# Optimization experiments

Measured on AMD Instinct MI355X. Metric: run time of the kernel, lower is better.

Reference implementation:

```python
import jax, jax.numpy as jnp
import numpy as np

N_NODES = 100000
N_EDGES = 640000


def _sage_conv(x, src, dst, w_agg, b, w_root, n_nodes):
    # mean aggregation of source features into destination nodes
    msgs = x[src]  # [E, D] gather
    summed = jax.ops.segment_sum(msgs, dst, num_segments=n_nodes)  # [N, D]
    deg = jax.ops.segment_sum(jnp.ones((src.shape[0],), dtype=x.dtype), dst,
                              num_segments=n_nodes)  # [N]
    mean = summed / jnp.clip(deg, 1.0)[:, None]  # isolated nodes -> 0
    # PyG SAGEConv: lin_l(agg) + lin_r(x); bias lives on lin_l
    return mean @ w_agg.T + b + x @ w_root.T


def setup_inputs() -> dict:
    key = jax.random.key(0)
    ks = jax.random.split(key, 8)
    d_in, d_hid, d_out = 128, 256, 64
    x = jax.random.normal(ks[0], (N_NODES, d_in), dtype=jnp.float32)
    edge_index = jax.random.randint(ks[1], (2, N_EDGES), 0, N_NODES, dtype=jnp.int64)
    s = 0.05
    return {
        "x": x,
        "edge_index": edge_index,
        "w1_agg": jax.random.normal(ks[2], (d_hid, d_in), dtype=jnp.float32) * s,
        "b1": jax.random.normal(ks[3], (d_hid,), dtype=jnp.float32) * s,
        "w1_root": jax.random.normal(ks[4], (d_hid, d_in), dtype=jnp.float32) * s,
        "w2_agg": jax.random.normal(ks[5], (d_out, d_hid), dtype=jnp.float32) * s,
        "b2": jax.random.normal(ks[6], (d_out,), dtype=jnp.float32) * s,
        "w2_root": jax.random.normal(ks[7], (d_out, d_hid), dtype=jnp.float32) * s,
    }


def reference(x, edge_index, w1_agg, b1, w1_root, w2_agg, b2, w2_root):
    src, dst = edge_index[0], edge_index[1]
    n = x.shape[0]
    h = _sage_conv(x, src, dst, w1_agg, b1, w1_root, n)
    h = jax.nn.relu(h)
    # dropout(p=0.5) is identity in eval mode
    h = _sage_conv(h, src, dst, w2_agg, b2, w2_root, n)
    return jax.nn.log_softmax(h, axis=1)
```

## Files before the change

kernel.cpp:

```cpp
#include <hip/hip_runtime.h>

#define N_NODES 100000
#define N_EDGES 640000
#define D_IN 128
#define D_HID 256
#define D_OUT 64

#define NROWPAD 100096
#define CAP 32

#define OB_CNT      0u
#define OB_BUCKET   401408u
#define OB_XQ       13201408u
#define OB_MEANQ    26013696u
#define OB_HB       38825984u
#define OB_ZRB      90075136u
#define OB_ZAQ      102887424u
#define OB_WCAT1    109293568u
#define OB_WCAT2    109424640u

typedef __attribute__((ext_vector_type(8))) short bf16x8;
typedef __attribute__((ext_vector_type(4))) float f32x4;
typedef __attribute__((ext_vector_type(2))) float f32x2;

__device__ __forceinline__ ushort f2bf(float f) {
    uint u = __float_as_uint(f);
    u += 0x7FFFu + ((u >> 16) & 1u);
    return (ushort)(u >> 16);
}
__device__ __forceinline__ float bf1(ushort u) { return __uint_as_float((uint)u << 16); }
__device__ __forceinline__ uchar f2q(float v) {
    return (uchar)(__builtin_amdgcn_cvt_pk_fp8_f32(v, v, 0, false) & 0xFF);
}
__device__ __forceinline__ uint pk8(float4 v) {
    uint q = (uint)__builtin_amdgcn_cvt_pk_fp8_f32(v.x, v.y, 0, false);
    return (uint)__builtin_amdgcn_cvt_pk_fp8_f32(v.z, v.w, (int)q, true);
}
__device__ __forceinline__ uint pkbf(float lo, float hi) {
    return (__float_as_uint(lo) >> 16) | (__float_as_uint(hi) & 0xFFFF0000u);
}


__global__ __launch_bounds__(256) void k_z(
    int* __restrict__ cnt,
    const float* __restrict__ w1a, const float* __restrict__ w1r,
    const float* __restrict__ w2r, const float* __restrict__ w2a,
    ushort* __restrict__ wcat1, ushort* __restrict__ wcat2)
{
    int b = blockIdx.x;
    if (b < 98) {
        int i = (b * 256 + threadIdx.x) * 4;
        *(int4*)(cnt + i) = make_int4(0, 0, 0, 0);
    } else {
        int i = (b - 98) * 256 + threadIdx.x;
        if (i < 65536) {
            int n = i >> 8, k = i & 255;
            float v = (k < 128) ? w1a[n * 128 + k] : w1r[n * 128 + (k - 128)];
            wcat1[i] = f2bf(v);
        } else {
            int j = i - 65536;
            int n = j >> 8, k = j & 255;
            float v = (n < 64) ? w2r[n * 256 + k] : w2a[(n - 64) * 256 + k];
            wcat2[j] = f2bf(v);
        }
    }
}


__global__ __launch_bounds__(256) void k_fc(
    const int* __restrict__ src, const int* __restrict__ dst,
    int* __restrict__ cnt, int* __restrict__ bucket,
    const float* __restrict__ x, uchar* __restrict__ xq)
{
    int b = blockIdx.x;
    if (b < 625) {
        int e = (b * 256 + threadIdx.x) * 4;
        int4 d = *(const int4*)(dst + e);
        int4 sv = *(const int4*)(src + e);
        int p0 = atomicAdd(&cnt[d.x], 1);
        int p1 = atomicAdd(&cnt[d.y], 1);
        int p2 = atomicAdd(&cnt[d.z], 1);
        int p3 = atomicAdd(&cnt[d.w], 1);
        if (p0 < CAP) bucket[(d.x << 5) + p0] = sv.x;
        if (p1 < CAP) bucket[(d.y << 5) + p1] = sv.y;
        if (p2 < CAP) bucket[(d.z << 5) + p2] = sv.z;
        if (p3 < CAP) bucket[(d.w << 5) + p3] = sv.w;
    } else {
        size_t i = ((size_t)(b - 625) * 256 + threadIdx.x) * 16;
        float4 v0 = *(const float4*)(x + i);
        float4 v1 = *(const float4*)(x + i + 4);
        float4 v2 = *(const float4*)(x + i + 8);
        float4 v3 = *(const float4*)(x + i + 12);
        uint4 q;
        q.x = pk8(v0); q.y = pk8(v1); q.z = pk8(v2); q.w = pk8(v3);
        *(uint4*)(xq + i) = q;
    }
}


__global__ __launch_bounds__(256) void k_gather(
    const uchar* __restrict__ xq, const int* __restrict__ cnt,
    const int* __restrict__ bucket, uchar* __restrict__ meanq)
{
    int tid = threadIdx.x;
    int node = blockIdx.x * 8 + (tid >> 5);
    int l = tid & 31;
    int g = l & 3, t = l >> 2;
    int nraw = cnt[node];
    int n = min(nraw, CAP);
    const int* cs = bucket + (node << 5);

    float a[16] = {};
    for (int j = 0; j < n; j += 4) {
        int jj = j + g;
        int ii = (jj < n) ? jj : 0;
        float w = (jj < n) ? 1.0f : 0.0f;
        int s = cs[ii];
        uint4 q = *(const uint4*)(xq + (size_t)s * D_IN + t * 16);
        f32x2 p;
        p = __builtin_amdgcn_cvt_pk_f32_fp8(q.x, false); a[0] += w*p.x; a[1] += w*p.y;
        p = __builtin_amdgcn_cvt_pk_f32_fp8(q.x, true);  a[2] += w*p.x; a[3] += w*p.y;
        p = __builtin_amdgcn_cvt_pk_f32_fp8(q.y, false); a[4] += w*p.x; a[5] += w*p.y;
        p = __builtin_amdgcn_cvt_pk_f32_fp8(q.y, true);  a[6] += w*p.x; a[7] += w*p.y;
        p = __builtin_amdgcn_cvt_pk_f32_fp8(q.z, false); a[8] += w*p.x; a[9] += w*p.y;
        p = __builtin_amdgcn_cvt_pk_f32_fp8(q.z, true);  a[10]+= w*p.x; a[11]+= w*p.y;
        p = __builtin_amdgcn_cvt_pk_f32_fp8(q.w, false); a[12]+= w*p.x; a[13]+= w*p.y;
        p = __builtin_amdgcn_cvt_pk_f32_fp8(q.w, true);  a[14]+= w*p.x; a[15]+= w*p.y;
    }

    float b[8];
    #pragma unroll
    for (int j = 0; j < 8; ++j) {
        int base = (j & 3) + 8 * (j >> 2);
        float mine = (l & 1) ? a[base + 4] : a[base];
        float send = (l & 1) ? a[base]     : a[base + 4];
        b[j] = mine + __shfl_xor(send, 1);
    }
    float c[4];
    #pragma unroll
    for (int j = 0; j < 4; ++j) {
        float mine = (l & 2) ? b[j + 4] : b[j];
        float send = (l & 2) ? b[j]     : b[j + 4];
        c[j] = mine + __shfl_xor(send, 2);
    }
    float id = 1.0f / fmaxf((float)nraw, 1.0f);
    uint q = (uint)__builtin_amdgcn_cvt_pk_fp8_f32(c[0] * id, c[1] * id, 0, false);
    q = (uint)__builtin_amdgcn_cvt_pk_fp8_f32(c[2] * id, c[3] * id, (int)q, true);
    *(uint*)(meanq + (size_t)node * D_IN + t * 16 + (l & 3) * 4) = q;
}


template<int MODE>
__global__ __launch_bounds__(256, 2) void k_gemm(
    const void* __restrict__ A0v, const void* __restrict__ A1v,
    const ushort* __restrict__ B,
    const float* __restrict__ bias,
    void* __restrict__ out0, void* __restrict__ out1)
{
    __shared__ char lds[32 * 1024];
    const int BB = (MODE == 0) ? 8192 : 16384;

    const int tid = threadIdx.x;
    const int lane = tid & 63;
    const int w = tid >> 6;
    const int wm = w >> 1, wn = w & 1;
    const int row0 = blockIdx.x * 128;
    const int col0 = blockIdx.y * 128;

    f32x4 acc[4][4] = {};

    for (int kt = 0; kt < 4; ++kt) {
        const int k0 = kt * 64;

        if (MODE == 0) {
            const uchar* asrc = (kt < 2) ? (const uchar*)A0v : (const uchar*)A1v;
            int kbyte = (kt & 1) * 64;
            #pragma unroll
            for (int i = 0; i < 2; ++i) {
                int elem = i * 256 + tid;
                int r = elem >> 2;
                int c4 = (elem & 3) ^ (r & 3);
                const uchar* gp = asrc + (size_t)(row0 + r) * 128 + kbyte + c4 * 16;
                __builtin_amdgcn_global_load_lds(
                    (const __attribute__((address_space(1))) void*)gp,
                    (__attribute__((address_space(3))) void*)&lds[i * 4096 + w * 1024],
                    16, 0, 0);
            }
        } else {
            const ushort* asrc = (const ushort*)A0v;
            #pragma unroll
            for (int i = 0; i < 4; ++i) {
                int elem = i * 256 + tid;
                int r = elem >> 3;
                int c8 = (elem & 7) ^ (r & 7);
                const ushort* gp = asrc + (size_t)(row0 + r) * 256 + k0 + c8 * 8;
                __builtin_amdgcn_global_load_lds(
                    (const __attribute__((address_space(1))) void*)gp,
                    (__attribute__((address_space(3))) void*)&lds[i * 4096 + w * 1024],
                    16, 0, 0);
            }
        }
        #pragma unroll
        for (int i = 0; i < 4; ++i) {
            int elem = i * 256 + tid;
            int r = elem >> 3;
            int c8 = (elem & 7) ^ (r & 7);
            const ushort* gp = B + (size_t)(col0 + r) * 256 + k0 + c8 * 8;
            __builtin_amdgcn_global_load_lds(
                (const __attribute__((address_space(1))) void*)gp,
                (__attribute__((address_space(3))) void*)&lds[BB + i * 4096 + w * 1024],
                16, 0, 0);
        }
        asm volatile("s_waitcnt vmcnt(0)" ::: "memory");
        __syncthreads();

        #pragma unroll
        for (int ks = 0; ks < 2; ++ks) {
            bf16x8 af[4], bfr[4];
            #pragma unroll
            for (int mi = 0; mi < 4; ++mi) {
                int r = wm * 64 + mi * 16 + (lane & 15);
                int g = lane >> 4;
                if (MODE == 0) {
                    int c4l = ks * 2 + (g >> 1);
                    int abyte = r * 64 + ((c4l ^ (r & 3)) << 4) + ((g & 1) << 3);
                    uint2 q = *(const uint2*)(lds + abyte);
                    f32x2 p0 = __builtin_amdgcn_cvt_pk_f32_fp8(q.x, false);
                    f32x2 p1 = __builtin_amdgcn_cvt_pk_f32_fp8(q.x, true);
                    f32x2 p2 = __builtin_amdgcn_cvt_pk_f32_fp8(q.y, false);
                    f32x2 p3 = __builtin_amdgcn_cvt_pk_f32_fp8(q.y, true);
                    uint4 u;
                    u.x = pkbf(p0.x, p0.y); u.y = pkbf(p1.x, p1.y);
                    u.z = pkbf(p2.x, p2.y); u.w = pkbf(p3.x, p3.y);
                    af[mi] = *(bf16x8*)&u;
                } else {
                    int c8 = ks * 4 + g;
                    int abyte = r * 128 + ((c8 ^ (r & 7)) << 4);
                    af[mi] = *(const bf16x8*)(lds + abyte);
                }
            }
            #pragma unroll
            for (int ni = 0; ni < 4; ++ni) {
                int r = wn * 64 + ni * 16 + (lane & 15);
                int c8 = ks * 4 + (lane >> 4);
                int byteoff = BB + r * 128 + ((c8 ^ (r & 7)) << 4);
                bfr[ni] = *(const bf16x8*)(lds + byteoff);
            }
            #pragma unroll
            for (int mi = 0; mi < 4; ++mi)
                #pragma unroll
                for (int ni = 0; ni < 4; ++ni)
                    acc[mi][ni] = __builtin_amdgcn_mfma_f32_16x16x32_bf16(
                        af[mi], bfr[ni], acc[mi][ni], 0, 0, 0);
        }
        __syncthreads();
    }

    const int orow_base = row0 + wm * 64;
    const int ocol_base = col0 + wn * 64;
    #pragma unroll
    for (int mi = 0; mi < 4; ++mi) {
        #pragma unroll
        for (int ni = 0; ni < 4; ++ni) {
            int ocol = ocol_base + ni * 16 + (lane & 15);
            #pragma unroll
            for (int r = 0; r < 4; ++r) {
                int orow = orow_base + mi * 16 + (lane >> 4) * 4 + r;
                float v = acc[mi][ni][r];
                if (MODE == 0) {
                    v = fmaxf(v + bias[ocol], 0.0f);
                    ((ushort*)out0)[(size_t)orow * 256 + ocol] = f2bf(v);
                } else {
                    if (ocol < 64)
                        ((ushort*)out0)[(size_t)orow * 64 + ocol] = f2bf(v + bias[ocol]);
                    else
                        ((uchar*)out1)[(size_t)orow * 64 + (ocol - 64)] = f2q(v);
                }
            }
        }
    }
}


__global__ __launch_bounds__(256) void k_final(
    const ushort* __restrict__ zrb, const uchar* __restrict__ zaq,
    const int* __restrict__ cnt, const int* __restrict__ bucket,
    float* __restrict__ out)
{
    int tid = threadIdx.x;
    int lane = tid & 63;
    int l = lane & 31;
    int node = blockIdx.x * 8 + (tid >> 5);
    int g = l & 7, t = l >> 3;
    int nraw = cnt[node];
    int n = min(nraw, CAP);
    const int* cs = bucket + (node << 5);

    float a[16] = {};
    for (int j = 0; j < n; j += 8) {
        int jj = j + g;
        int ii = (jj < n) ? jj : 0;
        float w = (jj < n) ? 1.0f : 0.0f;
        int s = cs[ii];
        uint4 q = *(const uint4*)(zaq + (size_t)s * 64 + t * 16);
        f32x2 p;
        p = __builtin_amdgcn_cvt_pk_f32_fp8(q.x, false); a[0] += w*p.x; a[1] += w*p.y;
        p = __builtin_amdgcn_cvt_pk_f32_fp8(q.x, true);  a[2] += w*p.x; a[3] += w*p.y;
        p = __builtin_amdgcn_cvt_pk_f32_fp8(q.y, false); a[4] += w*p.x; a[5] += w*p.y;
        p = __builtin_amdgcn_cvt_pk_f32_fp8(q.y, true);  a[6] += w*p.x; a[7] += w*p.y;
        p = __builtin_amdgcn_cvt_pk_f32_fp8(q.z, false); a[8] += w*p.x; a[9] += w*p.y;
        p = __builtin_amdgcn_cvt_pk_f32_fp8(q.z, true);  a[10]+= w*p.x; a[11]+= w*p.y;
        p = __builtin_amdgcn_cvt_pk_f32_fp8(q.w, false); a[12]+= w*p.x; a[13]+= w*p.y;
        p = __builtin_amdgcn_cvt_pk_f32_fp8(q.w, true);  a[14]+= w*p.x; a[15]+= w*p.y;
    }

    float b[8];
    #pragma unroll
    for (int j = 0; j < 8; ++j) {
        float mine = (l & 1) ? a[2*j+1] : a[2*j];
        float send = (l & 1) ? a[2*j]   : a[2*j+1];
        b[j] = mine + __shfl_xor(send, 1);
    }
    float c[4];
    #pragma unroll
    for (int j = 0; j < 4; ++j) {
        float mine = (l & 2) ? b[2*j+1] : b[2*j];
        float send = (l & 2) ? b[2*j]   : b[2*j+1];
        c[j] = mine + __shfl_xor(send, 2);
    }
    float m0 = (l & 4) ? c[1] : c[0];
    float s0 = (l & 4) ? c[0] : c[1];
    float e0 = m0 + __shfl_xor(s0, 4);
    float m1 = (l & 4) ? c[3] : c[2];
    float s1 = (l & 4) ? c[2] : c[3];
    float e1 = m1 + __shfl_xor(s1, 4);

    int c0 = t * 16 + (l & 7);
    float id = 1.0f / fmaxf((float)nraw, 1.0f);
    float v0 = e0 * id + bf1(zrb[(size_t)node * 64 + c0]);
    float v1 = e1 * id + bf1(zrb[(size_t)node * 64 + c0 + 8]);

    float m = fmaxf(v0, v1);
    #pragma unroll
    for (int o = 1; o < 32; o <<= 1) m = fmaxf(m, __shfl_xor(m, o));
    float ssum = __expf(v0 - m) + __expf(v1 - m);
    #pragma unroll
    for (int o = 1; o < 32; o <<= 1) ssum += __shfl_xor(ssum, o);
    float lse = m + __logf(ssum);

    out[(size_t)node * 64 + c0]     = v0 - lse;
    out[(size_t)node * 64 + c0 + 8] = v1 - lse;
}


extern "C" void kernel_launch(void* const* d_in, const int* in_sizes, int n_in,
                              void* d_out, int out_size, void* d_ws, size_t ws_size,
                              hipStream_t stream)
{
    const float* x   = (const float*)d_in[0];
    const int*   ei  = (const int*)d_in[1];
    const float* w1a = (const float*)d_in[2];
    const float* b1  = (const float*)d_in[3];
    const float* w1r = (const float*)d_in[4];
    const float* w2a = (const float*)d_in[5];
    const float* b2  = (const float*)d_in[6];
    const float* w2r = (const float*)d_in[7];
    float* out = (float*)d_out;

    char* ws = (char*)d_ws;
    const int* src = ei;
    const int* dst = ei + N_EDGES;

    int*    cnt       = (int*)(ws + OB_CNT);
    int*    bucket    = (int*)(ws + OB_BUCKET);
    uchar*  xq        = (uchar*)(ws + OB_XQ);
    uchar*  meanq     = (uchar*)(ws + OB_MEANQ);
    ushort* hb        = (ushort*)(ws + OB_HB);
    ushort* zrb       = (ushort*)(ws + OB_ZRB);
    uchar*  zaq       = (uchar*)(ws + OB_ZAQ);
    ushort* wcat1     = (ushort*)(ws + OB_WCAT1);
    ushort* wcat2     = (ushort*)(ws + OB_WCAT2);

    k_z<<<482, 256, 0, stream>>>(cnt, w1a, w1r, w2r, w2a, wcat1, wcat2);
    k_fc<<<3750, 256, 0, stream>>>(src, dst, cnt, bucket, x, xq);

    k_gather<<<12500, 256, 0, stream>>>(xq, cnt, bucket, meanq);

    dim3 g1(NROWPAD / 128, 2);
    k_gemm<0><<<g1, 256, 0, stream>>>((const void*)meanq, (const void*)xq,
                                      wcat1, b1, (void*)hb, nullptr);

    dim3 g2(NROWPAD / 128, 1);
    k_gemm<1><<<g2, 256, 0, stream>>>((const void*)hb, (const void*)hb,
                                      wcat2, b2, (void*)zrb, (void*)zaq);

    k_final<<<12500, 256, 0, stream>>>(zrb, zaq, cnt, bucket, out);
}
```

Baseline: 147.7 us.

## Transform-before-aggregate in layer 1, fusing bucket build into the first GEMM

Layer 1 now multiplies x by both weight matrices first, producing a 512-column output: root half in bf16 with bias, aggregate half in fp8. The mean aggregation then runs on the projected 256-wide fp8 features and fuses bias-added root, ReLU and the bf16 store of h. The edge bucketing atomics are folded into the GEMM kernel, which also reads fp32 x directly, dropping the separate x quantise pass and the layer-1 gather and GEMM launches. The cost is a gather over 256-wide rows instead of 128, plus more intermediate traffic for the 512-wide projection.

```diff
diff --git a/kernel.cpp b/kernel.cpp
--- a/kernel.cpp
+++ b/kernel.cpp
@@ -4,20 +4,19 @@
 #define N_EDGES 640000
 #define D_IN 128
 #define D_HID 256
-#define D_OUT 64
 
 #define NROWPAD 100096
 #define CAP 32
 
 #define OB_CNT      0u
 #define OB_BUCKET   401408u
-#define OB_XQ       13201408u
-#define OB_MEANQ    26013696u
-#define OB_HB       38825984u
-#define OB_ZRB      90075136u
-#define OB_ZAQ      102887424u
-#define OB_WCAT1    109293568u
-#define OB_WCAT2    109424640u
+#define OB_Z1R      13201408u
+#define OB_Z1A      64450560u
+#define OB_HB       90075136u
+#define OB_ZRB      141324288u
+#define OB_ZAQ      154136576u
+#define OB_WCAT1    160542720u
+#define OB_WCAT2    160673792u
 
 typedef __attribute__((ext_vector_type(8))) short bf16x8;
 typedef __attribute__((ext_vector_type(4))) float f32x4;
@@ -32,10 +31,6 @@
 __device__ __forceinline__ uchar f2q(float v) {
     return (uchar)(__builtin_amdgcn_cvt_pk_fp8_f32(v, v, 0, false) & 0xFF);
 }
-__device__ __forceinline__ uint pk8(float4 v) {
-    uint q = (uint)__builtin_amdgcn_cvt_pk_fp8_f32(v.x, v.y, 0, false);
-    return (uint)__builtin_amdgcn_cvt_pk_fp8_f32(v.z, v.w, (int)q, true);
-}
 __device__ __forceinline__ uint pkbf(float lo, float hi) {
     return (__float_as_uint(lo) >> 16) | (__float_as_uint(hi) & 0xFFFF0000u);
 }
@@ -43,7 +38,7 @@
 
 __global__ __launch_bounds__(256) void k_z(
     int* __restrict__ cnt,
-    const float* __restrict__ w1a, const float* __restrict__ w1r,
+    const float* __restrict__ w1r, const float* __restrict__ w1a,
     const float* __restrict__ w2r, const float* __restrict__ w2a,
     ushort* __restrict__ wcat1, ushort* __restrict__ wcat2)
 {
@@ -54,8 +49,8 @@
     } else {
         int i = (b - 98) * 256 + threadIdx.x;
         if (i < 65536) {
-            int n = i >> 8, k = i & 255;
-            float v = (k < 128) ? w1a[n * 128 + k] : w1r[n * 128 + (k - 128)];
+            int n = i >> 7, k = i & 127;
+            float v = (n < 256) ? w1r[n * 128 + k] : w1a[(n - 256) * 128 + k];
             wcat1[i] = f2bf(v);
         } else {
             int j = i - 65536;
@@ -67,45 +62,127 @@
 }
 
 
-__global__ __launch_bounds__(256) void k_fc(
+__global__ __launch_bounds__(256, 2) void k_big(
     const int* __restrict__ src, const int* __restrict__ dst,
     int* __restrict__ cnt, int* __restrict__ bucket,
-    const float* __restrict__ x, uchar* __restrict__ xq)
-{
-    int b = blockIdx.x;
-    if (b < 625) {
-        int e = (b * 256 + threadIdx.x) * 4;
-        int4 d = *(const int4*)(dst + e);
-        int4 sv = *(const int4*)(src + e);
-        int p0 = atomicAdd(&cnt[d.x], 1);
-        int p1 = atomicAdd(&cnt[d.y], 1);
-        int p2 = atomicAdd(&cnt[d.z], 1);
-        int p3 = atomicAdd(&cnt[d.w], 1);
-        if (p0 < CAP) bucket[(d.x << 5) + p0] = sv.x;
-        if (p1 < CAP) bucket[(d.y << 5) + p1] = sv.y;
-        if (p2 < CAP) bucket[(d.z << 5) + p2] = sv.z;
-        if (p3 < CAP) bucket[(d.w << 5) + p3] = sv.w;
-    } else {
-        size_t i = ((size_t)(b - 625) * 256 + threadIdx.x) * 16;
-        float4 v0 = *(const float4*)(x + i);
-        float4 v1 = *(const float4*)(x + i + 4);
-        float4 v2 = *(const float4*)(x + i + 8);
-        float4 v3 = *(const float4*)(x + i + 12);
-        uint4 q;
-        q.x = pk8(v0); q.y = pk8(v1); q.z = pk8(v2); q.w = pk8(v3);
-        *(uint4*)(xq + i) = q;
-    }
-}
-
-
-__global__ __launch_bounds__(256) void k_gather(
-    const uchar* __restrict__ xq, const int* __restrict__ cnt,
-    const int* __restrict__ bucket, uchar* __restrict__ meanq)
+    const float* __restrict__ x, const ushort* __restrict__ wcat1,
+    const float* __restrict__ b1,
+    ushort* __restrict__ z1r, uchar* __restrict__ z1a)
+{
+    __shared__ char lds[49152];
+
+    const int bb = blockIdx.x;
+    const int tid = threadIdx.x;
+
+    int e = bb * 205 + tid;
+    bool edge_ok = (tid < 205) && (e < N_EDGES);
+    int ed = edge_ok ? dst[e] : 0;
+    int es = edge_ok ? src[e] : 0;
+
+    const int bx = bb >> 2, by = bb & 3;
+    const int row0 = bx * 128;
+    const int col0 = by * 128;
+    const int lane = tid & 63;
+    const int w = tid >> 6;
+    const int wm = w >> 1, wn = w & 1;
+
+    f32x4 acc[4][4] = {};
+
+    for (int kt = 0; kt < 2; ++kt) {
+        #pragma unroll
+        for (int i = 0; i < 8; ++i) {
+            int elem = i * 256 + tid;
+            int r = elem >> 4;
+            int c = elem & 15;
+            int csrc = c ^ ((r & 7) << 1);
+            int rr = row0 + r; rr = rr < N_NODES ? rr : (N_NODES - 1);
+            const float* gp = x + (size_t)rr * 128 + kt * 64 + csrc * 4;
+            __builtin_amdgcn_global_load_lds(
+                (const __attribute__((address_space(1))) void*)gp,
+                (__attribute__((address_space(3))) void*)&lds[i * 4096 + w * 1024],
+                16, 0, 0);
+        }
+        #pragma unroll
+        for (int i = 0; i < 4; ++i) {
+            int elem = i * 256 + tid;
+            int r = elem >> 3;
+            int c8 = (elem & 7) ^ (r & 7);
+            const ushort* gp = wcat1 + (size_t)(col0 + r) * 128 + kt * 64 + c8 * 8;
+            __builtin_amdgcn_global_load_lds(
+                (const __attribute__((address_space(1))) void*)gp,
+                (__attribute__((address_space(3))) void*)&lds[32768 + i * 4096 + w * 1024],
+                16, 0, 0);
+        }
+        asm volatile("s_waitcnt vmcnt(0)" ::: "memory");
+        __syncthreads();
+
+        #pragma unroll
+        for (int ks = 0; ks < 2; ++ks) {
+            bf16x8 af[4], bfr[4];
+            #pragma unroll
+            for (int mi = 0; mi < 4; ++mi) {
+                int r = wm * 64 + mi * 16 + (lane & 15);
+                int g = lane >> 4;
+                int ct = ks * 8 + g * 2;
+                int base = r * 256 + ((ct ^ ((r & 7) << 1)) << 4);
+                f32x4 u0 = *(const f32x4*)(lds + base);
+                f32x4 u1 = *(const f32x4*)(lds + base + 16);
+                uint4 u;
+                u.x = pkbf(u0[0], u0[1]); u.y = pkbf(u0[2], u0[3]);
+                u.z = pkbf(u1[0], u1[1]); u.w = pkbf(u1[2], u1[3]);
+                af[mi] = *(bf16x8*)&u;
+            }
+            #pragma unroll
+            for (int ni = 0; ni < 4; ++ni) {
+                int r = wn * 64 + ni * 16 + (lane & 15);
+                int c8 = ks * 4 + (lane >> 4);
+                int byteoff = 32768 + r * 128 + ((c8 ^ (r & 7)) << 4);
+                bfr[ni] = *(const bf16x8*)(lds + byteoff);
+            }
+            #pragma unroll
+            for (int mi = 0; mi < 4; ++mi)
+                #pragma unroll
+                for (int ni = 0; ni < 4; ++ni)
+                    acc[mi][ni] = __builtin_amdgcn_mfma_f32_16x16x32_bf16(
+                        af[mi], bfr[ni], acc[mi][ni], 0, 0, 0);
+        }
+        __syncthreads();
+    }
+
+    int p = 0;
+    if (edge_ok) p = atomicAdd(&cnt[ed], 1);
+
+    const int orow_base = row0 + wm * 64;
+    #pragma unroll
+    for (int mi = 0; mi < 4; ++mi) {
+        #pragma unroll
+        for (int ni = 0; ni < 4; ++ni) {
+            int ocol = col0 + wn * 64 + ni * 16 + (lane & 15);
+            #pragma unroll
+            for (int r = 0; r < 4; ++r) {
+                int orow = orow_base + mi * 16 + (lane >> 4) * 4 + r;
+                float v = acc[mi][ni][r];
+                if (ocol < 256)
+                    z1r[(size_t)orow * 256 + ocol] = f2bf(v + b1[ocol]);
+                else
+                    z1a[(size_t)orow * 256 + (ocol - 256)] = f2q(v);
+            }
+        }
+    }
+
+    if (edge_ok && p < CAP) bucket[(ed << 5) + p] = es;
+}
+
+
+__global__ __launch_bounds__(256) void k_gatherh(
+    const uchar* __restrict__ z1a, const ushort* __restrict__ z1r,
+    const int* __restrict__ cnt, const int* __restrict__ bucket,
+    ushort* __restrict__ hb)
 {
     int tid = threadIdx.x;
-    int node = blockIdx.x * 8 + (tid >> 5);
-    int l = tid & 31;
-    int g = l & 3, t = l >> 2;
+    int node = blockIdx.x * 4 + (tid >> 6);
+    int l = tid & 63;
+    int g = l >> 4, t = l & 15;
     int nraw = cnt[node];
     int n = min(nraw, CAP);
     const int* cs = bucket + (node << 5);
@@ -116,7 +193,7 @@
         int ii = (jj < n) ? jj : 0;
         float w = (jj < n) ? 1.0f : 0.0f;
         int s = cs[ii];
-        uint4 q = *(const uint4*)(xq + (size_t)s * D_IN + t * 16);
+        uint4 q = *(const uint4*)(z1a + (size_t)s * 256 + t * 16);
         f32x2 p;
         p = __builtin_amdgcn_cvt_pk_f32_fp8(q.x, false); a[0] += w*p.x; a[1] += w*p.y;
         p = __builtin_amdgcn_cvt_pk_f32_fp8(q.x, true);  a[2] += w*p.x; a[3] += w*p.y;
@@ -132,83 +209,66 @@
     #pragma unroll
     for (int j = 0; j < 8; ++j) {
         int base = (j & 3) + 8 * (j >> 2);
-        float mine = (l & 1) ? a[base + 4] : a[base];
-        float send = (l & 1) ? a[base]     : a[base + 4];
-        b[j] = mine + __shfl_xor(send, 1);
+        float mine = (l & 16) ? a[base + 4] : a[base];
+        float send = (l & 16) ? a[base]     : a[base + 4];
+        b[j] = mine + __shfl_xor(send, 16);
     }
     float c[4];
     #pragma unroll
     for (int j = 0; j < 4; ++j) {
-        float mine = (l & 2) ? b[j + 4] : b[j];
-        float send = (l & 2) ? b[j]     : b[j + 4];
-        c[j] = mine + __shfl_xor(send, 2);
+        float mine = (l & 32) ? b[j + 4] : b[j];
+        float send = (l & 32) ? b[j]     : b[j + 4];
+        c[j] = mine + __shfl_xor(send, 32);
     }
     float id = 1.0f / fmaxf((float)nraw, 1.0f);
-    uint q = (uint)__builtin_amdgcn_cvt_pk_fp8_f32(c[0] * id, c[1] * id, 0, false);
-    q = (uint)__builtin_amdgcn_cvt_pk_fp8_f32(c[2] * id, c[3] * id, (int)q, true);
-    *(uint*)(meanq + (size_t)node * D_IN + t * 16 + (l & 3) * 4) = q;
-}
-
-
-template<int MODE>
-__global__ __launch_bounds__(256, 2) void k_gemm(
-    const void* __restrict__ A0v, const void* __restrict__ A1v,
-    const ushort* __restrict__ B,
-    const float* __restrict__ bias,
-    void* __restrict__ out0, void* __restrict__ out1)
+    size_t off = (size_t)node * 256 + t * 16 + g * 4;
+    ushort4 zr = *(const ushort4*)(z1r + off);
+    ushort4 o;
+    o.x = f2bf(fmaxf(c[0] * id + bf1(zr.x), 0.0f));
+    o.y = f2bf(fmaxf(c[1] * id + bf1(zr.y), 0.0f));
+    o.z = f2bf(fmaxf(c[2] * id + bf1(zr.z), 0.0f));
+    o.w = f2bf(fmaxf(c[3] * id + bf1(zr.w), 0.0f));
+    *(ushort4*)(hb + off) = o;
+}
+
+
+__global__ __launch_bounds__(256, 2) void k_gemm2(
+    const ushort* __restrict__ hb, const ushort* __restrict__ B,
+    const float* __restrict__ b2,
+    ushort* __restrict__ zrb, uchar* __restrict__ zaq)
 {
     __shared__ char lds[32 * 1024];
-    const int BB = (MODE == 0) ? 8192 : 16384;
 
     const int tid = threadIdx.x;
     const int lane = tid & 63;
     const int w = tid >> 6;
     const int wm = w >> 1, wn = w & 1;
     const int row0 = blockIdx.x * 128;
-    const int col0 = blockIdx.y * 128;
 
     f32x4 acc[4][4] = {};
 
     for (int kt = 0; kt < 4; ++kt) {
         const int k0 = kt * 64;
-
-        if (MODE == 0) {
-            const uchar* asrc = (kt < 2) ? (const uchar*)A0v : (const uchar*)A1v;
-            int kbyte = (kt & 1) * 64;
-            #pragma unroll
-            for (int i = 0; i < 2; ++i) {
-                int elem = i * 256 + tid;
-                int r = elem >> 2;
-                int c4 = (elem & 3) ^ (r & 3);
-                const uchar* gp = asrc + (size_t)(row0 + r) * 128 + kbyte + c4 * 16;
-                __builtin_amdgcn_global_load_lds(
-                    (const __attribute__((address_space(1))) void*)gp,
-                    (__attribute__((address_space(3))) void*)&lds[i * 4096 + w * 1024],
-                    16, 0, 0);
-            }
-        } else {
-            const ushort* asrc = (const ushort*)A0v;
-            #pragma unroll
-            for (int i = 0; i < 4; ++i) {
-                int elem = i * 256 + tid;
-                int r = elem >> 3;
-                int c8 = (elem & 7) ^ (r & 7);
-                const ushort* gp = asrc + (size_t)(row0 + r) * 256 + k0 + c8 * 8;
-                __builtin_amdgcn_global_load_lds(
-                    (const __attribute__((address_space(1))) void*)gp,
-                    (__attribute__((address_space(3))) void*)&lds[i * 4096 + w * 1024],
-                    16, 0, 0);
-            }
-        }
         #pragma unroll
         for (int i = 0; i < 4; ++i) {
             int elem = i * 256 + tid;
             int r = elem >> 3;
             int c8 = (elem & 7) ^ (r & 7);
-            const ushort* gp = B + (size_t)(col0 + r) * 256 + k0 + c8 * 8;
+            const ushort* gp = hb + (size_t)(row0 + r) * 256 + k0 + c8 * 8;
             __builtin_amdgcn_global_load_lds(
                 (const __attribute__((address_space(1))) void*)gp,
-                (__attribute__((address_space(3))) void*)&lds[BB + i * 4096 + w * 1024],
+                (__attribute__((address_space(3))) void*)&lds[i * 4096 + w * 1024],
+                16, 0, 0);
+        }
+        #pragma unroll
+        for (int i = 0; i < 4; ++i) {
+            int elem = i * 256 + tid;
+            int r = elem >> 3;
+            int c8 = (elem & 7) ^ (r & 7);
+            const ushort* gp = B + (size_t)r * 256 + k0 + c8 * 8;
+            __builtin_amdgcn_global_load_lds(
+                (const __attribute__((address_space(1))) void*)gp,
+                (__attribute__((address_space(3))) void*)&lds[16384 + i * 4096 + w * 1024],
                 16, 0, 0);
         }
         asm volatile("s_waitcnt vmcnt(0)" ::: "memory");
@@ -220,31 +280,14 @@
             #pragma unroll
             for (int mi = 0; mi < 4; ++mi) {
                 int r = wm * 64 + mi * 16 + (lane & 15);
-                int g = lane >> 4;
-                if (MODE == 0) {
-                    int c4l = ks * 2 + (g >> 1);
-                    int abyte = r * 64 + ((c4l ^ (r & 3)) << 4) + ((g & 1) << 3);
-                    uint2 q = *(const uint2*)(lds + abyte);
-                    f32x2 p0 = __builtin_amdgcn_cvt_pk_f32_fp8(q.x, false);
-                    f32x2 p1 = __builtin_amdgcn_cvt_pk_f32_fp8(q.x, true);
-                    f32x2 p2 = __builtin_amdgcn_cvt_pk_f32_fp8(q.y, false);
-                    f32x2 p3 = __builtin_amdgcn_cvt_pk_f32_fp8(q.y, true);
-                    uint4 u;
-                    u.x = pkbf(p0.x, p0.y); u.y = pkbf(p1.x, p1.y);
-                    u.z = pkbf(p2.x, p2.y); u.w = pkbf(p3.x, p3.y);
-                    af[mi] = *(bf16x8*)&u;
-                } else {
-                    int c8 = ks * 4 + g;
-                    int abyte = r * 128 + ((c8 ^ (r & 7)) << 4);
-                    af[mi] = *(const bf16x8*)(lds + abyte);
-                }
+                int c8 = ks * 4 + (lane >> 4);
+                af[mi] = *(const bf16x8*)(lds + r * 128 + ((c8 ^ (r & 7)) << 4));
             }
             #pragma unroll
             for (int ni = 0; ni < 4; ++ni) {
                 int r = wn * 64 + ni * 16 + (lane & 15);
                 int c8 = ks * 4 + (lane >> 4);
-                int byteoff = BB + r * 128 + ((c8 ^ (r & 7)) << 4);
-                bfr[ni] = *(const bf16x8*)(lds + byteoff);
+                bfr[ni] = *(const bf16x8*)(lds + 16384 + r * 128 + ((c8 ^ (r & 7)) << 4));
             }
             #pragma unroll
             for (int mi = 0; mi < 4; ++mi)
@@ -257,7 +300,7 @@
     }
 
     const int orow_base = row0 + wm * 64;
-    const int ocol_base = col0 + wn * 64;
+    const int ocol_base = wn * 64;
     #pragma unroll
     for (int mi = 0; mi < 4; ++mi) {
         #pragma unroll
@@ -267,15 +310,10 @@
             for (int r = 0; r < 4; ++r) {
                 int orow = orow_base + mi * 16 + (lane >> 4) * 4 + r;
                 float v = acc[mi][ni][r];
-                if (MODE == 0) {
-                    v = fmaxf(v + bias[ocol], 0.0f);
-                    ((ushort*)out0)[(size_t)orow * 256 + ocol] = f2bf(v);
-                } else {
-                    if (ocol < 64)
-                        ((ushort*)out0)[(size_t)orow * 64 + ocol] = f2bf(v + bias[ocol]);
-                    else
-                        ((uchar*)out1)[(size_t)orow * 64 + (ocol - 64)] = f2q(v);
-                }
+                if (ocol < 64)
+                    zrb[(size_t)orow * 64 + ocol] = f2bf(v + b2[ocol]);
+                else
+                    zaq[(size_t)orow * 64 + (ocol - 64)] = f2q(v);
             }
         }
     }
@@ -371,28 +409,19 @@
     const int* src = ei;
     const int* dst = ei + N_EDGES;
 
-    int*    cnt       = (int*)(ws + OB_CNT);
-    int*    bucket    = (int*)(ws + OB_BUCKET);
-    uchar*  xq        = (uchar*)(ws + OB_XQ);
-    uchar*  meanq     = (uchar*)(ws + OB_MEANQ);
-    ushort* hb        = (ushort*)(ws + OB_HB);
-    ushort* zrb       = (ushort*)(ws + OB_ZRB);
-    uchar*  zaq       = (uchar*)(ws + OB_ZAQ);
-    ushort* wcat1     = (ushort*)(ws + OB_WCAT1);
-    ushort* wcat2     = (ushort*)(ws + OB_WCAT2);
-
-    k_z<<<482, 256, 0, stream>>>(cnt, w1a, w1r, w2r, w2a, wcat1, wcat2);
-    k_fc<<<3750, 256, 0, stream>>>(src, dst, cnt, bucket, x, xq);
-
-    k_gather<<<12500, 256, 0, stream>>>(xq, cnt, bucket, meanq);
-
-    dim3 g1(NROWPAD / 128, 2);
-    k_gemm<0><<<g1, 256, 0, stream>>>((const void*)meanq, (const void*)xq,
-                                      wcat1, b1, (void*)hb, nullptr);
-
-    dim3 g2(NROWPAD / 128, 1);
-    k_gemm<1><<<g2, 256, 0, stream>>>((const void*)hb, (const void*)hb,
-                                      wcat2, b2, (void*)zrb, (void*)zaq);
-
+    int*    cnt    = (int*)(ws + OB_CNT);
+    int*    bucket = (int*)(ws + OB_BUCKET);
+    ushort* z1r    = (ushort*)(ws + OB_Z1R);
+    uchar*  z1a    = (uchar*)(ws + OB_Z1A);
+    ushort* hb     = (ushort*)(ws + OB_HB);
+    ushort* zrb    = (ushort*)(ws + OB_ZRB);
+    uchar*  zaq    = (uchar*)(ws + OB_ZAQ);
+    ushort* wcat1  = (ushort*)(ws + OB_WCAT1);
+    ushort* wcat2  = (ushort*)(ws + OB_WCAT2);
+
+    k_z<<<482, 256, 0, stream>>>(cnt, w1r, w1a, w2r, w2a, wcat1, wcat2);
+    k_big<<<3128, 256, 0, stream>>>(src, dst, cnt, bucket, x, wcat1, b1, z1r, z1a);
+    k_gatherh<<<25000, 256, 0, stream>>>(z1a, z1r, cnt, bucket, hb);
+    k_gemm2<<<782, 256, 0, stream>>>(hb, wcat2, b2, zrb, zaq);
     k_final<<<12500, 256, 0, stream>>>(zrb, zaq, cnt, bucket, out);
 }
```

Measured after the change: 187.6 us. 1.27x slower.
